# Performance work log

Hardware: AMD Instinct MI355X
Metric: run time of the kernel (lower is better)

The kernel has to match this reference:

```python
import jax, jax.numpy as jnp
import numpy as np

K_TOP = 10  # module init k


def setup_inputs() -> dict:
    key = jax.random.key(0)
    k1, k2 = jax.random.split(key)
    B, C, H, W = 32, 512, 64, 64
    num_item = 100
    x = jax.random.normal(k1, (B, C, H, W), dtype=jnp.float32)
    # mempool initialized uniform(-stdv, stdv) with stdv = 1/sqrt(dim), as in init_memory
    stdv = 1.0 / np.sqrt(C)
    mempool = jax.random.uniform(k2, (num_item, C), minval=-stdv, maxval=stdv, dtype=jnp.float32)
    return {"x": x, "mempool": mempool}


def reference(x, mempool):
    B, C, H, W = x.shape
    # permute to channels-last, flatten spatial+batch -> queries [N, C]
    q = x.transpose(0, 2, 3, 1).reshape(-1, C)
    # attention over memory items: F.linear(query, mempool) == q @ mempool.T
    att = jax.nn.softmax(q @ mempool.T, axis=1)  # [N, num_item]
    val, idx = jax.lax.top_k(att, K_TOP)          # [N, k]
    val = jax.nn.softmax(val, axis=1)             # renormalize over top-k
    N = q.shape[0]
    # scatter renormalized weights back into a sparse attention matrix
    att_sp = jnp.zeros_like(att).at[jnp.arange(N)[:, None], idx].set(val)
    # reconstruct: F.linear(att, mempool.T) == att @ mempool
    out = (att_sp @ mempool).reshape(B, H, W, C).transpose(0, 3, 1, 2)
    # diversity loss on the memory pool
    m = mempool.shape[0]
    cosim = (mempool @ mempool.T) * 0.5
    off_diag = cosim * (1.0 - jnp.eye(m, dtype=cosim.dtype))
    loss = jnp.mean(jnp.abs(off_diag))
    return (out, loss)
```

## Files before the change

### kernel.cpp

```cpp
#include <hip/hip_runtime.h>
#include <math.h>

#define NITEM 100
#define CDIM 512
#define HW 4096
#define KTOP 10

typedef __attribute__((ext_vector_type(8))) short bf16x8;
typedef __attribute__((ext_vector_type(4))) float f32x4;

__device__ inline unsigned short bf16u(float f) {
  unsigned int u = __float_as_uint(f);
  u += 0x7fffu + ((u >> 16) & 1u);
  return (unsigned short)(u >> 16);
}

__global__ __launch_bounds__(128, 2) void logits_topk(
    const float* __restrict__ x, const float* __restrict__ mp,
    unsigned short* __restrict__ Wd)
{
  __shared__ float smem[12928];
  float* qs = smem;
  float* ms = smem + 4096;
  float* ls = smem;

  const int t   = threadIdx.x;
  const int tc  = t & 7;
  const int tr  = t >> 3;
  const int n0  = blockIdx.x * 128;
  const int b   = n0 >> 12;
  const int sp0 = n0 & (HW - 1);
  const float* xb = x + (size_t)b * CDIM * HW + sp0;

  const int h    = t >> 2;
  const int G    = ((h & 3) << 3) | (h >> 2);
  const int mcol = (G << 2) | (t & 3);
  const float* mrow = mp + (size_t)(t < NITEM ? t : 0) * CDIM;

  float acc[8][16];
  #pragma unroll
  for (int j = 0; j < 8; ++j)
    #pragma unroll
    for (int i = 0; i < 16; ++i) acc[j][i] = 0.f;

  const int wv = t >> 6, ln = t & 63;

  for (int kt = 0; kt < 16; ++kt) {
    const int k0 = kt * 32;
    __syncthreads();
    #pragma unroll
    for (int i = 0; i < 8; ++i) {
      int e  = i * 512 + wv * 256 + ln * 4;
      int kk = e >> 7, q = e & 127;
      float4 v = *(const float4*)(xb + (size_t)(k0 + kk) * HW + q);
      *(float4*)(qs + e) = v;
    }
    #pragma unroll
    for (int g = 0; g < 8; ++g) {
      float4 v = make_float4(0.f, 0.f, 0.f, 0.f);
      if (t < NITEM) v = *(const float4*)(mrow + k0 + 4 * g);
      ms[(4*g + 0) * 128 + mcol] = v.x;
      ms[(4*g + 1) * 128 + mcol] = v.y;
      ms[(4*g + 2) * 128 + mcol] = v.z;
      ms[(4*g + 3) * 128 + mcol] = v.w;
    }
    __syncthreads();
    #pragma unroll 2
    for (int kk = 0; kk < 32; ++kk) {
      const float* qr = qs + kk * 128;
      const float* mr = ms + kk * 128;
      float4 qA = *(const float4*)(qr + 4 * tr);
      float4 qB = *(const float4*)(qr + 64 + 4 * tr);
      float4 m0 = *(const float4*)(mr + ((0*8 + tc) << 2));
      float4 m1 = *(const float4*)(mr + ((1*8 + tc) << 2));
      float4 m2 = *(const float4*)(mr + ((2*8 + tc) << 2));
      float4 m3 = *(const float4*)(mr + ((3*8 + tc) << 2));
      float qv[8]  = {qA.x,qA.y,qA.z,qA.w,qB.x,qB.y,qB.z,qB.w};
      float mv[16] = {m0.x,m0.y,m0.z,m0.w, m1.x,m1.y,m1.z,m1.w,
                      m2.x,m2.y,m2.z,m2.w, m3.x,m3.y,m3.z,m3.w};
      #pragma unroll
      for (int j = 0; j < 8; ++j)
        #pragma unroll
        for (int i = 0; i < 16; ++i)
          acc[j][i] = __builtin_fmaf(qv[j], mv[i], acc[j][i]);
    }
  }

  __syncthreads();
  #pragma unroll
  for (int j = 0; j < 8; ++j) {
    int row = (j < 4) ? (4 * tr + j) : (64 + 4 * tr + (j - 4));
    #pragma unroll
    for (int i = 0; i < 4; ++i)
      #pragma unroll
      for (int jj = 0; jj < 4; ++jj) {
        int it = 16 * tc + 4 * i + jj;
        if (it < 101) ls[row * 101 + it] = acc[j][4 * i + jj];
      }
  }
  __syncthreads();

  {
    float* lr = ls + t * 101;
    float mx = -INFINITY;
    #pragma unroll 4
    for (int j = 0; j < NITEM; ++j) mx = fmaxf(mx, lr[j]);
    float Z = 0.f;
    #pragma unroll 4
    for (int j = 0; j < NITEM; ++j) Z += expf(lr[j] - mx);
    float att[KTOP]; int id[KTOP];
    #pragma unroll 1
    for (int s = 0; s < KTOP; ++s) {
      float vm = -INFINITY; int im = 0;
      #pragma unroll 4
      for (int j = 0; j < NITEM; ++j) {
        float v = lr[j];
        if (v > vm) { vm = v; im = j; }
      }
      lr[im] = -INFINITY;
      att[s] = expf(vm - mx) / Z;
      id[s]  = im;
    }
    float s2 = 0.f, w[KTOP];
    #pragma unroll
    for (int s = 0; s < KTOP; ++s) { w[s] = expf(att[s] - att[0]); s2 += w[s]; }
    float inv = 1.f / s2;
    unsigned short* wrow = Wd + (size_t)(n0 + t) * 112;
    float4 z4 = make_float4(0.f, 0.f, 0.f, 0.f);
    #pragma unroll
    for (int f = 0; f < 14; ++f) *(float4*)(wrow + 8 * f) = z4;
    #pragma unroll
    for (int s = 0; s < KTOP; ++s) wrow[id[s]] = bf16u(w[s] * inv);
  }
}

__global__ __launch_bounds__(256, 2) void recon(
    const float* __restrict__ mp, const unsigned short* __restrict__ Wd,
    float* __restrict__ out)
{
  __shared__ unsigned short Ash[128 * 136];
  __shared__ unsigned short Bsh[128 * 136];
  const int t  = threadIdx.x;
  const int ct = blockIdx.x & 3, nt = blockIdx.x >> 2;
  const int c0 = ct * 128, n0 = nt * 128;
  const int b  = n0 >> 12, sp0 = n0 & (HW - 1);

  #pragma unroll
  for (int j = 0; j < 13; ++j) {
    int task = t + 256 * j;
    if (task < 3200) {
      int k = task >> 5, c4 = (task & 31) << 2;
      float4 v = *(const float4*)(mp + (size_t)k * CDIM + c0 + c4);
      Ash[(c4 + 0) * 136 + k] = bf16u(v.x);
      Ash[(c4 + 1) * 136 + k] = bf16u(v.y);
      Ash[(c4 + 2) * 136 + k] = bf16u(v.z);
      Ash[(c4 + 3) * 136 + k] = bf16u(v.w);
    }
  }
  {
    int c = t >> 1, hf = t & 1;
    unsigned int* A32 = (unsigned int*)Ash;
    #pragma unroll
    for (int j = 0; j < 9; ++j) { int k = 100 + 2 * (hf * 9 + j); A32[(c * 136 + k) >> 1] = 0u; }
  }
  {
    int n = t >> 1, hf = t & 1;
    #pragma unroll
    for (int j = 0; j < 7; ++j) {
      int f = hf * 7 + j;
      *(bf16x8*)(Bsh + n * 136 + 8 * f) = *(const bf16x8*)(Wd + (size_t)(n0 + n) * 112 + 8 * f);
    }
    unsigned int* B32 = (unsigned int*)Bsh;
    #pragma unroll
    for (int j = 0; j < 6; ++j) { int k = 112 + 2 * (hf * 6 + j); B32[(n * 136 + k) >> 1] = 0u; }
  }
  __syncthreads();

  const int w = t >> 6, l = t & 63;
  const int arow = l & 15, kg = l >> 4;
  f32x4 acc[2][8];
  #pragma unroll
  for (int cr = 0; cr < 2; ++cr)
    #pragma unroll
    for (int n = 0; n < 8; ++n) acc[cr][n] = (f32x4){0.f, 0.f, 0.f, 0.f};

  #pragma unroll
  for (int ks = 0; ks < 4; ++ks) {
    bf16x8 a0 = *(bf16x8*)(Ash + ((2*w + 0) * 16 + arow) * 136 + ks * 32 + kg * 8);
    bf16x8 a1 = *(bf16x8*)(Ash + ((2*w + 1) * 16 + arow) * 136 + ks * 32 + kg * 8);
    #pragma unroll
    for (int nn = 0; nn < 8; ++nn) {
      bf16x8 bb = *(bf16x8*)(Bsh + (nn * 16 + arow) * 136 + ks * 32 + kg * 8);
      acc[0][nn] = __builtin_amdgcn_mfma_f32_16x16x32_bf16(a0, bb, acc[0][nn], 0, 0, 0);
      acc[1][nn] = __builtin_amdgcn_mfma_f32_16x16x32_bf16(a1, bb, acc[1][nn], 0, 0, 0);
    }
  }

  float* ob = out + (size_t)b * CDIM * HW + sp0;
  #pragma unroll
  for (int cr = 0; cr < 2; ++cr) {
    #pragma unroll
    for (int nn = 0; nn < 8; ++nn) {
      int ncol = nn * 16 + arow;
      #pragma unroll
      for (int j = 0; j < 4; ++j) {
        int cc = c0 + (2*w + cr) * 16 + kg * 4 + j;
        ob[(size_t)cc * HW + ncol] = acc[cr][nn][j];
      }
    }
  }
}

__global__ void loss_partial(const float* __restrict__ mp, float* __restrict__ part)
{
  __shared__ float mi[CDIM];
  __shared__ float red[4];
  const int i = blockIdx.x;
  const int t = threadIdx.x;
  for (int k = t; k < CDIM; k += 256) mi[k] = mp[i * CDIM + k];
  __syncthreads();
  float v = 0.f;
  if (t < NITEM && t != i) {
    const float* mj = mp + t * CDIM;
    float d = 0.f;
    #pragma unroll 8
    for (int k = 0; k < CDIM; ++k) d += mi[k] * mj[k];
    v = fabsf(0.5f * d);
  }
  #pragma unroll
  for (int o = 32; o > 0; o >>= 1) v += __shfl_down(v, o, 64);
  if ((t & 63) == 0) red[t >> 6] = v;
  __syncthreads();
  if (t == 0) part[i] = red[0] + red[1] + red[2] + red[3];
}

__global__ void loss_final(const float* __restrict__ part, float* __restrict__ out_loss)
{
  if (threadIdx.x == 0) {
    float s = 0.f;
    for (int i = 0; i < NITEM; ++i) s += part[i];
    *out_loss = s / (float)(NITEM * NITEM);
  }
}

extern "C" void kernel_launch(void* const* d_in, const int* in_sizes, int n_in,
                              void* d_out, int out_size, void* d_ws, size_t ws_size,
                              hipStream_t stream) {
  const float* x  = (const float*)d_in[0];
  const float* mp = (const float*)d_in[1];
  float* out = (float*)d_out;
  unsigned short* Wd = (unsigned short*)d_ws;
  float* part = (float*)((char*)d_ws + (size_t)131072 * 112 * 2);

  logits_topk<<<1024, 128, 0, stream>>>(x, mp, Wd);
  recon<<<4096, 256, 0, stream>>>(mp, Wd, out);
  loss_partial<<<NITEM, 256, 0, stream>>>(mp, part);
  loss_final<<<1, 64, 0, stream>>>(part, out + (out_size - 1));
}
```

Measured before the change: 427.3 us.

## Distribute logits and top-k across 16-lane groups with shuffle reductions

The logits/top-k kernel now uses 256 threads per block. Each 16-lane group owns 8 query rows, and each lane holds 7 memory items in registers. The serial per-thread softmax and top-k scan over a 100-entry shared-memory row is replaced by shuffle-based argmax and sum reductions within each 16-lane group, which removes the logits staging through LDS. Global loads are issued before the barrier to overlap with the previous tile. Each lane writes a packed 16-byte chunk of the bf16 weight row directly. This costs more threads, more shuffle traffic and more redundant exp work, and uses the faster but less accurate __expf.

```diff
diff --git a/kernel.cpp b/kernel.cpp
--- a/kernel.cpp
+++ b/kernel.cpp
@@ -15,122 +15,131 @@
   return (unsigned short)(u >> 16);
 }
 
-__global__ __launch_bounds__(128, 2) void logits_topk(
+__global__ __launch_bounds__(256, 4) void logits_topk(
     const float* __restrict__ x, const float* __restrict__ mp,
     unsigned short* __restrict__ Wd)
 {
-  __shared__ float smem[12928];
-  float* qs = smem;
-  float* ms = smem + 4096;
-  float* ls = smem;
+  __shared__ float qs[32 * 128];
+  __shared__ float ms[32 * 128];
 
   const int t   = threadIdx.x;
-  const int tc  = t & 7;
-  const int tr  = t >> 3;
+  const int tc  = t & 15;
+  const int trg = t >> 4;
   const int n0  = blockIdx.x * 128;
   const int b   = n0 >> 12;
   const int sp0 = n0 & (HW - 1);
   const float* xb = x + (size_t)b * CDIM * HW + sp0;
 
-  const int h    = t >> 2;
-  const int G    = ((h & 3) << 3) | (h >> 2);
-  const int mcol = (G << 2) | (t & 3);
-  const float* mrow = mp + (size_t)(t < NITEM ? t : 0) * CDIM;
-
-  float acc[8][16];
-  #pragma unroll
-  for (int j = 0; j < 8; ++j)
-    #pragma unroll
-    for (int i = 0; i < 16; ++i) acc[j][i] = 0.f;
-
-  const int wv = t >> 6, ln = t & 63;
+  const int item = t & 127;
+  const int half = t >> 7;
+  const float* mrow = mp + (size_t)(item < NITEM ? item : 0) * CDIM + 16 * half;
+
+  float acc[8][7];
+  #pragma unroll
+  for (int r = 0; r < 8; ++r)
+    #pragma unroll
+    for (int j = 0; j < 7; ++j) acc[r][j] = 0.f;
 
   for (int kt = 0; kt < 16; ++kt) {
     const int k0 = kt * 32;
+    float4 qv[4];
+    #pragma unroll
+    for (int j = 0; j < 4; ++j) {
+      int task = t + 256 * j;
+      int kk = task >> 5, c4 = (task & 31) << 2;
+      qv[j] = *(const float4*)(xb + (size_t)(k0 + kk) * HW + c4);
+    }
+    float4 mv4[4];
+    #pragma unroll
+    for (int u = 0; u < 4; ++u)
+      mv4[u] = *(const float4*)(mrow + k0 + 4 * u);
     __syncthreads();
     #pragma unroll
-    for (int i = 0; i < 8; ++i) {
-      int e  = i * 512 + wv * 256 + ln * 4;
-      int kk = e >> 7, q = e & 127;
-      float4 v = *(const float4*)(xb + (size_t)(k0 + kk) * HW + q);
-      *(float4*)(qs + e) = v;
-    }
-    #pragma unroll
-    for (int g = 0; g < 8; ++g) {
-      float4 v = make_float4(0.f, 0.f, 0.f, 0.f);
-      if (t < NITEM) v = *(const float4*)(mrow + k0 + 4 * g);
-      ms[(4*g + 0) * 128 + mcol] = v.x;
-      ms[(4*g + 1) * 128 + mcol] = v.y;
-      ms[(4*g + 2) * 128 + mcol] = v.z;
-      ms[(4*g + 3) * 128 + mcol] = v.w;
+    for (int j = 0; j < 4; ++j)
+      *(float4*)(qs + 4 * (t + 256 * j)) = qv[j];
+    #pragma unroll
+    for (int u = 0; u < 4; ++u) {
+      ms[(16 * half + 4 * u + 0) * 128 + item] = mv4[u].x;
+      ms[(16 * half + 4 * u + 1) * 128 + item] = mv4[u].y;
+      ms[(16 * half + 4 * u + 2) * 128 + item] = mv4[u].z;
+      ms[(16 * half + 4 * u + 3) * 128 + item] = mv4[u].w;
     }
     __syncthreads();
     #pragma unroll 2
     for (int kk = 0; kk < 32; ++kk) {
-      const float* qr = qs + kk * 128;
-      const float* mr = ms + kk * 128;
-      float4 qA = *(const float4*)(qr + 4 * tr);
-      float4 qB = *(const float4*)(qr + 64 + 4 * tr);
-      float4 m0 = *(const float4*)(mr + ((0*8 + tc) << 2));
-      float4 m1 = *(const float4*)(mr + ((1*8 + tc) << 2));
-      float4 m2 = *(const float4*)(mr + ((2*8 + tc) << 2));
-      float4 m3 = *(const float4*)(mr + ((3*8 + tc) << 2));
-      float qv[8]  = {qA.x,qA.y,qA.z,qA.w,qB.x,qB.y,qB.z,qB.w};
-      float mv[16] = {m0.x,m0.y,m0.z,m0.w, m1.x,m1.y,m1.z,m1.w,
-                      m2.x,m2.y,m2.z,m2.w, m3.x,m3.y,m3.z,m3.w};
-      #pragma unroll
-      for (int j = 0; j < 8; ++j)
+      const float* qr = qs + kk * 128 + 8 * trg;
+      const float* mr = ms + kk * 128 + tc;
+      float4 qa = *(const float4*)(qr);
+      float4 qb = *(const float4*)(qr + 4);
+      float mm[7] = {mr[0], mr[16], mr[32], mr[48], mr[64], mr[80], mr[96]};
+      float qq[8] = {qa.x, qa.y, qa.z, qa.w, qb.x, qb.y, qb.z, qb.w};
+      #pragma unroll
+      for (int r = 0; r < 8; ++r)
         #pragma unroll
-        for (int i = 0; i < 16; ++i)
-          acc[j][i] = __builtin_fmaf(qv[j], mv[i], acc[j][i]);
-    }
-  }
-
-  __syncthreads();
-  #pragma unroll
-  for (int j = 0; j < 8; ++j) {
-    int row = (j < 4) ? (4 * tr + j) : (64 + 4 * tr + (j - 4));
-    #pragma unroll
-    for (int i = 0; i < 4; ++i)
-      #pragma unroll
-      for (int jj = 0; jj < 4; ++jj) {
-        int it = 16 * tc + 4 * i + jj;
-        if (it < 101) ls[row * 101 + it] = acc[j][4 * i + jj];
-      }
-  }
-  __syncthreads();
-
-  {
-    float* lr = ls + t * 101;
-    float mx = -INFINITY;
-    #pragma unroll 4
-    for (int j = 0; j < NITEM; ++j) mx = fmaxf(mx, lr[j]);
-    float Z = 0.f;
-    #pragma unroll 4
-    for (int j = 0; j < NITEM; ++j) Z += expf(lr[j] - mx);
+        for (int j = 0; j < 7; ++j)
+          acc[r][j] = __builtin_fmaf(qq[r], mm[j], acc[r][j]);
+    }
+  }
+
+  const int baserow = n0 + 8 * trg;
+  #pragma unroll 1
+  for (int r = 0; r < 8; ++r) {
+    float* la = acc[r];
     float att[KTOP]; int id[KTOP];
+    float mx = 0.f, Z = 0.f;
     #pragma unroll 1
     for (int s = 0; s < KTOP; ++s) {
-      float vm = -INFINITY; int im = 0;
-      #pragma unroll 4
-      for (int j = 0; j < NITEM; ++j) {
-        float v = lr[j];
-        if (v > vm) { vm = v; im = j; }
-      }
-      lr[im] = -INFINITY;
-      att[s] = expf(vm - mx) / Z;
-      id[s]  = im;
-    }
+      float bv = -INFINITY; int bi = 0x7fffffff;
+      #pragma unroll
+      for (int j = 0; j < 7; ++j) {
+        bool valid = (j < 6) || (tc < 4);
+        float v = valid ? la[j] : -INFINITY;
+        if (v > bv) { bv = v; bi = tc + 16 * j; }
+      }
+      #pragma unroll
+      for (int d = 1; d < 16; d <<= 1) {
+        float ov = __shfl_xor(bv, d, 16);
+        int   oi = __shfl_xor(bi, d, 16);
+        if (ov > bv || (ov == bv && oi < bi)) { bv = ov; bi = oi; }
+      }
+      if (s == 0) {
+        mx = bv;
+        float zp = 0.f;
+        #pragma unroll
+        for (int j = 0; j < 7; ++j) {
+          bool valid = (j < 6) || (tc < 4);
+          zp += valid ? __expf(la[j] - mx) : 0.f;
+        }
+        #pragma unroll
+        for (int d = 1; d < 16; d <<= 1) zp += __shfl_xor(zp, d, 16);
+        Z = zp;
+      }
+      att[s] = bv; id[s] = bi;
+      if ((bi & 15) == tc) la[bi >> 4] = -INFINITY;
+    }
+    float invZ = 1.f / Z;
+    float p0 = invZ;
     float s2 = 0.f, w[KTOP];
     #pragma unroll
-    for (int s = 0; s < KTOP; ++s) { w[s] = expf(att[s] - att[0]); s2 += w[s]; }
-    float inv = 1.f / s2;
-    unsigned short* wrow = Wd + (size_t)(n0 + t) * 112;
-    float4 z4 = make_float4(0.f, 0.f, 0.f, 0.f);
-    #pragma unroll
-    for (int f = 0; f < 14; ++f) *(float4*)(wrow + 8 * f) = z4;
-    #pragma unroll
-    for (int s = 0; s < KTOP; ++s) wrow[id[s]] = bf16u(w[s] * inv);
+    for (int s = 0; s < KTOP; ++s) {
+      float p = __expf(att[s] - mx) * invZ;
+      float e = __expf(p - p0);
+      w[s] = e; s2 += e;
+    }
+    float inv2 = 1.f / s2;
+    unsigned int zz[4] = {0u, 0u, 0u, 0u};
+    #pragma unroll
+    for (int s = 0; s < KTOP; ++s) {
+      if ((id[s] >> 3) == tc) {
+        int pos = id[s] & 7;
+        unsigned int hw = (unsigned int)bf16u(w[s] * inv2);
+        zz[pos >> 1] |= hw << (16 * (pos & 1));
+      }
+    }
+    if (tc < 14) {
+      uint4 o; o.x = zz[0]; o.y = zz[1]; o.z = zz[2]; o.w = zz[3];
+      *(uint4*)(Wd + (size_t)(baserow + r) * 112 + 8 * tc) = o;
+    }
   }
 }
 
@@ -252,7 +261,7 @@
   unsigned short* Wd = (unsigned short*)d_ws;
   float* part = (float*)((char*)d_ws + (size_t)131072 * 112 * 2);
 
-  logits_topk<<<1024, 128, 0, stream>>>(x, mp, Wd);
+  logits_topk<<<1024, 256, 0, stream>>>(x, mp, Wd);
   recon<<<4096, 256, 0, stream>>>(mp, Wd, out);
   loss_partial<<<NITEM, 256, 0, stream>>>(mp, part);
   loss_final<<<1, 64, 0, stream>>>(part, out + (out_size - 1));
```

Result: slower. 766.7 us (+79.4%).
